# Optimization experiments

Measured on AMD Instinct MI355X. Metric: run time of the kernel, lower is better.

Reference implementation:

```python
import jax, jax.numpy as jnp
import numpy as np

_MAX_SQRT_GRADIENT = 1000.0
NUM_HEADS = 16


@jax.custom_vjp
def sqrt_bound(x):
    return jnp.sqrt(x)

def _sb_fwd(x):
    return jnp.sqrt(x), x

def _sb_bwd(x, g):
    return (g / jnp.sqrt(jnp.clip(4.0 * x, 1.0 / _MAX_SQRT_GRADIENT**2)),)

sqrt_bound.defvjp(_sb_fwd, _sb_bwd)


def block_diag_linear(x, w):
    # x: [..., H*I], w: [H, I, J]
    H, I, J = w.shape
    xb = x.reshape(x.shape[:-1] + (H, I))
    y = jnp.einsum('bshi,hij->bshj', xb, w)
    return y.reshape(x.shape[:-1] + (H * J,))


def self_att_pool(h, num_heads):
    # h: [B, S, D]; attention over S, then max over S with keepdims
    n_state = h.shape[-1] // num_heads
    scores = jnp.matmul(h, jnp.swapaxes(h, -2, -1)) * (1.0 / np.sqrt(n_state))
    attn = jax.nn.softmax(scores, axis=-1)              # [B, S, S]
    pooled = jnp.matmul(attn, h)                        # [B, S, D]
    return jnp.max(pooled, axis=-2, keepdims=True)      # [B, 1, D]


def setup_inputs() -> dict:
    key = jax.random.key(0)
    k1, k2, k3, k4 = jax.random.split(key, 4)
    B, S, D = 4, 4096, 2048
    H = NUM_HEADS
    bw = D // H  # 128
    std = np.sqrt(1.0 / bw)
    x = jax.random.normal(k1, (B, S, D), dtype=jnp.float32)
    h = jax.random.normal(k2, (B, S, D), dtype=jnp.float32)
    w_in = jax.random.normal(k3, (H, bw, bw), dtype=jnp.float32) * std
    w_a = jax.random.normal(k4, (H, bw, bw), dtype=jnp.float32) * std
    # rnn_param_init: uniform in [min_r^2+eps, max_r^2+eps], 0.5*log, then softplus-inverse of -t
    rng = np.random.default_rng(0)
    eps = 1e-8
    u = rng.uniform(0.9**2 + eps, 0.999**2 + eps, size=(D,)).astype(np.float32)
    t = 0.5 * np.log(u)
    a_param = jnp.asarray(np.log(np.exp(-t) - 1.0).astype(np.float32))
    return {"x": x, "h": h, "w_in": w_in, "w_a": w_a, "a_param": a_param}


def reference(x, h, w_in, w_a, a_param):
    gate_x = jax.nn.sigmoid(block_diag_linear(x, w_in))
    gate_a = jax.nn.sigmoid(block_diag_linear(x, w_a))
    log_a = -8.0 * jax.nn.softplus(a_param) * gate_a     # [B, S, D]
    a = jnp.exp(log_a)
    gated_x = x * gate_x
    normalized_x = gated_x * sqrt_bound(1.0 - jnp.exp(2.0 * log_a))
    h_pooled = self_att_pool(h, NUM_HEADS)               # [B, 1, D]
    return a * h_pooled + normalized_x
```

## Files before the change

kernel.cpp:

```cpp
#include <hip/hip_runtime.h>
#include <hip/hip_bf16.h>
#include <cstdint>

typedef _Float16 f16;
typedef _Float16 f16x4 __attribute__((ext_vector_type(4)));
typedef _Float16 f16x8 __attribute__((ext_vector_type(8)));
typedef float f32x4 __attribute__((ext_vector_type(4)));

#define B_ 4
#define S_ 4096
#define D_ 2048
#define NH 16
#define BW 128

__global__ __launch_bounds__(256) void cvt_kernel(const float* __restrict__ h,
                                                  f16* __restrict__ hf,
                                                  f16* __restrict__ hT) {
    __shared__ f16 tile[64][72];
    int s0 = blockIdx.y * 64;
    int d0 = blockIdx.x * 64;
    int tid = threadIdx.x;
    int r  = tid >> 4;
    int c4 = (tid & 15) * 4;
    #pragma unroll
    for (int rr = r; rr < 64; rr += 16) {
        f32x4 v = *(const f32x4*)(h + (size_t)(s0 + rr) * D_ + d0 + c4);
        f16x4 o;
        o[0] = (f16)v[0]; o[1] = (f16)v[1]; o[2] = (f16)v[2]; o[3] = (f16)v[3];
        *(f16x4*)(hf + (size_t)(s0 + rr) * D_ + d0 + c4) = o;
        tile[rr][c4 + 0] = o[0]; tile[rr][c4 + 1] = o[1];
        tile[rr][c4 + 2] = o[2]; tile[rr][c4 + 3] = o[3];
    }
    __syncthreads();
    #pragma unroll
    for (int dd = r; dd < 64; dd += 16) {
        f16x4 o;
        o[0] = tile[c4 + 0][dd]; o[1] = tile[c4 + 1][dd];
        o[2] = tile[c4 + 2][dd]; o[3] = tile[c4 + 3][dd];
        *(f16x4*)(hT + (size_t)(d0 + dd) * S_ + s0 + c4) = o;
    }
}

__device__ __forceinline__ unsigned f2ord(float f) {
    unsigned u = __float_as_uint(f);
    return (u & 0x80000000u) ? ~u : (u | 0x80000000u);
}

template<int EPI>
__global__ __launch_bounds__(256) void gemm_nt(const f16* __restrict__ A,
                                               const f16* __restrict__ Bm,
                                               float* __restrict__ C,
                                               unsigned* __restrict__ hp,
                                               int M, int N, int K, float alpha) {
    __shared__ f16 lA[128 * 32];
    __shared__ f16 lB[128 * 32];
    int tid  = threadIdx.x;
    int m0   = blockIdx.y * 128;
    int n0   = blockIdx.x * 128;
    int wave = tid >> 6;
    int lane = tid & 63;
    int wr   = (wave >> 1) * 64;
    int wc   = (wave & 1) * 64;
    int l15  = lane & 15;
    int quad = lane >> 4;

    const f16* aSrc = A + (size_t)(m0 + (tid >> 2)) * K + (tid & 3) * 8;
    const f16* bSrc = Bm + (size_t)(n0 + (tid >> 2)) * K + (tid & 3) * 8;
    size_t rowStep = (size_t)64 * K;

    f32x4 acc[4][4];
    #pragma unroll
    for (int i = 0; i < 4; i++)
        #pragma unroll
        for (int j = 0; j < 4; j++) acc[i][j] = (f32x4)0.0f;

    for (int k0 = 0; k0 < K; k0 += 32) {
        __builtin_amdgcn_global_load_lds(
            (const __attribute__((address_space(1))) void*)(aSrc),
            (__attribute__((address_space(3))) void*)(lA + tid * 8), 16, 0, 0);
        __builtin_amdgcn_global_load_lds(
            (const __attribute__((address_space(1))) void*)(aSrc + rowStep),
            (__attribute__((address_space(3))) void*)(lA + 2048 + tid * 8), 16, 0, 0);
        __builtin_amdgcn_global_load_lds(
            (const __attribute__((address_space(1))) void*)(bSrc),
            (__attribute__((address_space(3))) void*)(lB + tid * 8), 16, 0, 0);
        __builtin_amdgcn_global_load_lds(
            (const __attribute__((address_space(1))) void*)(bSrc + rowStep),
            (__attribute__((address_space(3))) void*)(lB + 2048 + tid * 8), 16, 0, 0);
        __syncthreads();

        f16x8 af[4], bf[4];
        #pragma unroll
        for (int i = 0; i < 4; i++) {
            af[i] = *(const f16x8*)(lA + (wr + i * 16 + l15) * 32 + quad * 8);
            bf[i] = *(const f16x8*)(lB + (wc + i * 16 + l15) * 32 + quad * 8);
        }
        #pragma unroll
        for (int i = 0; i < 4; i++)
            #pragma unroll
            for (int j = 0; j < 4; j++)
                acc[i][j] = __builtin_amdgcn_mfma_f32_16x16x32_f16(af[i], bf[j], acc[i][j], 0, 0, 0);
        __syncthreads();
        aSrc += 32; bSrc += 32;
    }

    if (EPI == 0) {
        #pragma unroll
        for (int i = 0; i < 4; i++) {
            int row = m0 + wr + i * 16 + quad * 4;
            #pragma unroll
            for (int j = 0; j < 4; j++) {
                int col = n0 + wc + j * 16 + l15;
                float* cp = C + (size_t)row * N + col;
                #pragma unroll
                for (int r = 0; r < 4; r++) cp[(size_t)r * N] = alpha * acc[i][j][r];
            }
        }
    } else {
        #pragma unroll
        for (int j = 0; j < 4; j++) {
            int col = n0 + wc + j * 16 + l15;
            float m = acc[0][j][0];
            #pragma unroll
            for (int i = 0; i < 4; i++)
                #pragma unroll
                for (int r = 0; r < 4; r++) m = fmaxf(m, acc[i][j][r]);
            atomicMax(hp + col, f2ord(m));
        }
    }
}

__global__ __launch_bounds__(256) void softmax_kernel(const float* __restrict__ scores,
                                                      f16* __restrict__ attn) {
    int row = blockIdx.x;
    int tid = threadIdx.x;
    const float* src = scores + (size_t)row * S_;
    f32x4 v[4];
    float m = -3.4e38f;
    #pragma unroll
    for (int j = 0; j < 4; j++) {
        v[j] = *(const f32x4*)(src + tid * 4 + j * 1024);
        #pragma unroll
        for (int e = 0; e < 4; e++) m = fmaxf(m, v[j][e]);
    }
    #pragma unroll
    for (int o = 32; o > 0; o >>= 1) m = fmaxf(m, __shfl_xor(m, o, 64));
    __shared__ float sm[4];
    __shared__ float ss[4];
    int wave = tid >> 6, lane = tid & 63;
    if (lane == 0) sm[wave] = m;
    __syncthreads();
    m = fmaxf(fmaxf(sm[0], sm[1]), fmaxf(sm[2], sm[3]));
    float sum = 0.f;
    #pragma unroll
    for (int j = 0; j < 4; j++)
        #pragma unroll
        for (int e = 0; e < 4; e++) { v[j][e] = __expf(v[j][e] - m); sum += v[j][e]; }
    #pragma unroll
    for (int o = 32; o > 0; o >>= 1) sum += __shfl_xor(sum, o, 64);
    if (lane == 0) ss[wave] = sum;
    __syncthreads();
    sum = ss[0] + ss[1] + ss[2] + ss[3];
    float inv = 1.0f / sum;
    f16* dst = attn + (size_t)row * S_;
    #pragma unroll
    for (int j = 0; j < 4; j++) {
        f16x4 o;
        #pragma unroll
        for (int e = 0; e < 4; e++) o[e] = (f16)(v[j][e] * inv);
        *(f16x4*)(dst + tid * 4 + j * 1024) = o;
    }
}

__global__ __launch_bounds__(256, 2) void final_kernel(const float* __restrict__ x,
                                                       const float* __restrict__ w_in,
                                                       const float* __restrict__ w_a,
                                                       const float* __restrict__ a_param,
                                                       const unsigned* __restrict__ hp_u,
                                                       float* __restrict__ out) {
    __shared__ float xs[8 * 2048];
    int wg = blockIdx.x;
    int b  = wg >> 9;
    int s0 = (wg & 511) * 8;
    int tid = threadIdx.x;
    const float* xbase = x + ((size_t)b * S_ + s0) * D_;
    {
        int r  = tid >> 5;
        int c0 = (tid & 31) * 4;
        #pragma unroll
        for (int it = 0; it < 16; it++) {
            int c = c0 + it * 128;
            *(f32x4*)(xs + r * 2048 + c) = *(const f32x4*)(xbase + (size_t)r * D_ + c);
        }
    }
    __syncthreads();

    int hd = tid >> 4;
    int j0 = (tid & 15) * 8;
    const float* wi  = w_in + hd * (BW * BW) + j0;
    const float* wa  = w_a  + hd * (BW * BW) + j0;
    const float* xsh = xs + hd * 128;

    float accx[8][8], acca[8][8];
    #pragma unroll
    for (int jj = 0; jj < 8; jj++)
        #pragma unroll
        for (int r = 0; r < 8; r++) { accx[jj][r] = 0.f; acca[jj][r] = 0.f; }

    for (int i = 0; i < 128; i += 4) {
        f32x4 xr[8];
        #pragma unroll
        for (int r = 0; r < 8; r++) xr[r] = *(const f32x4*)(xsh + r * 2048 + i);
        #pragma unroll
        for (int k = 0; k < 4; k++) {
            f32x4 wv0 = *(const f32x4*)(wi + (i + k) * 128);
            f32x4 wv1 = *(const f32x4*)(wi + (i + k) * 128 + 4);
            f32x4 wa0 = *(const f32x4*)(wa + (i + k) * 128);
            f32x4 wa1 = *(const f32x4*)(wa + (i + k) * 128 + 4);
            #pragma unroll
            for (int jj = 0; jj < 8; jj++) {
                float wiv = (jj < 4) ? wv0[jj] : wv1[jj - 4];
                float wav = (jj < 4) ? wa0[jj] : wa1[jj - 4];
                #pragma unroll
                for (int r = 0; r < 8; r++) {
                    accx[jj][r] = fmaf(xr[r][k], wiv, accx[jj][r]);
                    acca[jj][r] = fmaf(xr[r][k], wav, acca[jj][r]);
                }
            }
        }
    }

    float n8sp[8], hpv[8];
    #pragma unroll
    for (int jj = 0; jj < 8; jj++) {
        int d = hd * 128 + j0 + jj;
        n8sp[jj] = -8.f * log1pf(__expf(a_param[d]));
        unsigned u = hp_u[b * D_ + d];
        unsigned bits = (u >> 31) ? (u ^ 0x80000000u) : ~u;
        hpv[jj] = __uint_as_float(bits);
    }
    float* obase = out + ((size_t)b * S_ + s0) * D_ + hd * 128 + j0;
    #pragma unroll
    for (int r = 0; r < 8; r++) {
        f32x4 o0, o1;
        #pragma unroll
        for (int jj = 0; jj < 8; jj++) {
            float gx = 1.f / (1.f + __expf(-accx[jj][r]));
            float ga = 1.f / (1.f + __expf(-acca[jj][r]));
            float a  = __expf(n8sp[jj] * ga);
            float ns = sqrtf(fmaxf(1.f - a * a, 0.f));
            float xv = xs[r * 2048 + hd * 128 + j0 + jj];
            float val = a * hpv[jj] + xv * gx * ns;
            if (jj < 4) o0[jj] = val; else o1[jj - 4] = val;
        }
        *(f32x4*)(obase + (size_t)r * D_) = o0;
        *(f32x4*)(obase + (size_t)r * D_ + 4) = o1;
    }
}

extern "C" void kernel_launch(void* const* d_in, const int* in_sizes, int n_in,
                              void* d_out, int out_size, void* d_ws, size_t ws_size,
                              hipStream_t stream) {
    const float* x       = (const float*)d_in[0];
    const float* h       = (const float*)d_in[1];
    const float* w_in    = (const float*)d_in[2];
    const float* w_a     = (const float*)d_in[3];
    const float* a_param = (const float*)d_in[4];
    float* out = (float*)d_out;

    char* ws = (char*)d_ws;
    f16*      hf     = (f16*)ws;
    f16*      hT     = (f16*)(ws + ((size_t)16 << 20));
    float*    scores = (float*)(ws + ((size_t)32 << 20));
    f16*      attn   = (f16*)(ws + ((size_t)96 << 20));
    unsigned* hp     = (unsigned*)(ws + ((size_t)128 << 20));

    hipMemsetAsync(hp, 0, (size_t)B_ * D_ * sizeof(unsigned), stream);

    const float scale = 0.08838834764831845f;
    for (int b = 0; b < B_; b++) {
        const f16* hfc = hf;
        const f16* hTc = hT;
        const float* hb = h + (size_t)b * S_ * D_;
        cvt_kernel<<<dim3(D_ / 64, S_ / 64), 256, 0, stream>>>(hb, hf, hT);
        gemm_nt<0><<<dim3(S_ / 128, S_ / 128), 256, 0, stream>>>(
            hfc, hfc, scores, nullptr, S_, S_, D_, scale);
        softmax_kernel<<<dim3(S_), 256, 0, stream>>>(scores, attn);
        gemm_nt<1><<<dim3(D_ / 128, S_ / 128), 256, 0, stream>>>(
            attn, hTc, nullptr, hp + b * D_, S_, D_, S_, 1.0f);
    }
    final_kernel<<<dim3((B_ * S_) / 8), 256, 0, stream>>>(x, w_in, w_a, a_param, hp, out);
}
```

Before: 1.541 ms.

## Move gate projections to MFMA and store attention scores in fp16

Replaces the fp32 FMA block-diagonal gate kernel with an MFMA kernel. It stages pre-transposed fp16 weights, prepared once per call, and fp16-converted x tiles in LDS, one workgroup per 256 rows and one head. Separately, the QK^T GEMM now writes fp16 scores and softmax reads them, halving the traffic of the large scores buffer. The cost is lower precision: x is rounded to fp16 both for the gates and for the output term, the scores lose precision, and the new epilogue's per-element stores are less vectorized.

```diff
diff --git a/kernel.cpp b/kernel.cpp
--- a/kernel.cpp
+++ b/kernel.cpp
@@ -41,6 +41,24 @@
     }
 }
 
+__global__ __launch_bounds__(256) void prep_wT(const float* __restrict__ w,
+                                               f16* __restrict__ wT) {
+    int hd = blockIdx.x;
+    const float* src = w + hd * 16384;
+    f16* dst = wT + hd * 16384;
+    int tid = threadIdx.x;
+    int j0 = (tid & 31) * 4;
+    #pragma unroll
+    for (int p = 0; p < 16; p++) {
+        int i = (tid >> 5) + p * 8;
+        f32x4 v = *(const f32x4*)(src + i * 128 + j0);
+        int kc = i >> 5, il = i & 31;
+        #pragma unroll
+        for (int e = 0; e < 4; e++)
+            dst[kc * 4096 + (j0 + e) * 32 + il] = (f16)v[e];
+    }
+}
+
 __device__ __forceinline__ unsigned f2ord(float f) {
     unsigned u = __float_as_uint(f);
     return (u & 0x80000000u) ? ~u : (u | 0x80000000u);
@@ -49,7 +67,7 @@
 template<int EPI>
 __global__ __launch_bounds__(256) void gemm_nt(const f16* __restrict__ A,
                                                const f16* __restrict__ Bm,
-                                               float* __restrict__ C,
+                                               void* __restrict__ C,
                                                unsigned* __restrict__ hp,
                                                int M, int N, int K, float alpha) {
     __shared__ f16 lA[128 * 32];
@@ -105,15 +123,16 @@
     }
 
     if (EPI == 0) {
+        f16* Cf = (f16*)C;
         #pragma unroll
         for (int i = 0; i < 4; i++) {
             int row = m0 + wr + i * 16 + quad * 4;
             #pragma unroll
             for (int j = 0; j < 4; j++) {
                 int col = n0 + wc + j * 16 + l15;
-                float* cp = C + (size_t)row * N + col;
+                f16* cp = Cf + (size_t)row * N + col;
                 #pragma unroll
-                for (int r = 0; r < 4; r++) cp[(size_t)r * N] = alpha * acc[i][j][r];
+                for (int r = 0; r < 4; r++) cp[(size_t)r * N] = (f16)(alpha * acc[i][j][r]);
             }
         }
     } else {
@@ -130,19 +149,21 @@
     }
 }
 
-__global__ __launch_bounds__(256) void softmax_kernel(const float* __restrict__ scores,
+__global__ __launch_bounds__(256) void softmax_kernel(const f16* __restrict__ scores,
                                                       f16* __restrict__ attn) {
     int row = blockIdx.x;
     int tid = threadIdx.x;
-    const float* src = scores + (size_t)row * S_;
-    f32x4 v[4];
+    const f16* src = scores + (size_t)row * S_;
+    float v[16];
+    #pragma unroll
+    for (int j = 0; j < 2; j++) {
+        f16x8 raw = *(const f16x8*)(src + tid * 8 + j * 2048);
+        #pragma unroll
+        for (int e = 0; e < 8; e++) v[j * 8 + e] = (float)raw[e];
+    }
     float m = -3.4e38f;
     #pragma unroll
-    for (int j = 0; j < 4; j++) {
-        v[j] = *(const f32x4*)(src + tid * 4 + j * 1024);
-        #pragma unroll
-        for (int e = 0; e < 4; e++) m = fmaxf(m, v[j][e]);
-    }
+    for (int e = 0; e < 16; e++) m = fmaxf(m, v[e]);
     #pragma unroll
     for (int o = 32; o > 0; o >>= 1) m = fmaxf(m, __shfl_xor(m, o, 64));
     __shared__ float sm[4];
@@ -153,9 +174,7 @@
     m = fmaxf(fmaxf(sm[0], sm[1]), fmaxf(sm[2], sm[3]));
     float sum = 0.f;
     #pragma unroll
-    for (int j = 0; j < 4; j++)
-        #pragma unroll
-        for (int e = 0; e < 4; e++) { v[j][e] = __expf(v[j][e] - m); sum += v[j][e]; }
+    for (int e = 0; e < 16; e++) { v[e] = __expf(v[e] - m); sum += v[e]; }
     #pragma unroll
     for (int o = 32; o > 0; o >>= 1) sum += __shfl_xor(sum, o, 64);
     if (lane == 0) ss[wave] = sum;
@@ -164,97 +183,111 @@
     float inv = 1.0f / sum;
     f16* dst = attn + (size_t)row * S_;
     #pragma unroll
+    for (int j = 0; j < 2; j++) {
+        f16x8 o;
+        #pragma unroll
+        for (int e = 0; e < 8; e++) o[e] = (f16)(v[j * 8 + e] * inv);
+        *(f16x8*)(dst + tid * 8 + j * 2048) = o;
+    }
+}
+
+__global__ __launch_bounds__(512, 1) void final2_kernel(
+    const float* __restrict__ x, const f16* __restrict__ wTi,
+    const f16* __restrict__ wTa, const float* __restrict__ a_param,
+    const unsigned* __restrict__ hp_u, float* __restrict__ out) {
+    __shared__ f16 xs[4 * 256 * 32];
+    __shared__ f16 lwi[16384];
+    __shared__ f16 lwa[16384];
+    int tid  = threadIdx.x;
+    int hd   = blockIdx.y;
+    int row0 = blockIdx.x * 256;
+    int b    = row0 >> 12;
+    int wave = tid >> 6, lane = tid & 63;
+
+    const f16* wsi = wTi + hd * 16384;
+    const f16* wsa = wTa + hd * 16384;
+    #pragma unroll
+    for (int c = 0; c < 4; c++) {
+        int off = (wave * 4 + c) * 512 + lane * 8;
+        __builtin_amdgcn_global_load_lds(
+            (const __attribute__((address_space(1))) void*)(wsi + off),
+            (__attribute__((address_space(3))) void*)(lwi + off), 16, 0, 0);
+        __builtin_amdgcn_global_load_lds(
+            (const __attribute__((address_space(1))) void*)(wsa + off),
+            (__attribute__((address_space(3))) void*)(lwa + off), 16, 0, 0);
+    }
+
+    {
+        int rr   = tid >> 4;
+        int col8 = (tid & 15) * 8;
+        int kc = col8 >> 5, cl = col8 & 31;
+        const float* xb = x + (size_t)row0 * D_ + hd * 128;
+        #pragma unroll
+        for (int it = 0; it < 8; it++) {
+            int row = it * 32 + rr;
+            f32x4 v0 = *(const f32x4*)(xb + (size_t)row * D_ + col8);
+            f32x4 v1 = *(const f32x4*)(xb + (size_t)row * D_ + col8 + 4);
+            f16x8 o;
+            o[0] = (f16)v0[0]; o[1] = (f16)v0[1]; o[2] = (f16)v0[2]; o[3] = (f16)v0[3];
+            o[4] = (f16)v1[0]; o[5] = (f16)v1[1]; o[6] = (f16)v1[2]; o[7] = (f16)v1[3];
+            *(f16x8*)(xs + kc * 8192 + row * 32 + cl) = o;
+        }
+    }
+    __syncthreads();
+
+    int wr = (wave >> 1) * 64;
+    int wc = (wave & 1) * 64;
+    int l15 = lane & 15, quad = lane >> 4;
+
+    f32x4 ai[4][4], aa[4][4];
+    #pragma unroll
+    for (int i = 0; i < 4; i++)
+        #pragma unroll
+        for (int j = 0; j < 4; j++) { ai[i][j] = (f32x4)0.0f; aa[i][j] = (f32x4)0.0f; }
+
+    #pragma unroll
+    for (int ks = 0; ks < 4; ks++) {
+        f16x8 af[4], bi[4], ba[4];
+        #pragma unroll
+        for (int i = 0; i < 4; i++)
+            af[i] = *(const f16x8*)(xs + ks * 8192 + (wr + i * 16 + l15) * 32 + quad * 8);
+        #pragma unroll
+        for (int j = 0; j < 4; j++) {
+            bi[j] = *(const f16x8*)(lwi + ks * 4096 + (wc + j * 16 + l15) * 32 + quad * 8);
+            ba[j] = *(const f16x8*)(lwa + ks * 4096 + (wc + j * 16 + l15) * 32 + quad * 8);
+        }
+        #pragma unroll
+        for (int i = 0; i < 4; i++)
+            #pragma unroll
+            for (int j = 0; j < 4; j++) {
+                ai[i][j] = __builtin_amdgcn_mfma_f32_16x16x32_f16(af[i], bi[j], ai[i][j], 0, 0, 0);
+                aa[i][j] = __builtin_amdgcn_mfma_f32_16x16x32_f16(af[i], ba[j], aa[i][j], 0, 0, 0);
+            }
+    }
+
+    #pragma unroll
     for (int j = 0; j < 4; j++) {
-        f16x4 o;
-        #pragma unroll
-        for (int e = 0; e < 4; e++) o[e] = (f16)(v[j][e] * inv);
-        *(f16x4*)(dst + tid * 4 + j * 1024) = o;
-    }
-}
-
-__global__ __launch_bounds__(256, 2) void final_kernel(const float* __restrict__ x,
-                                                       const float* __restrict__ w_in,
-                                                       const float* __restrict__ w_a,
-                                                       const float* __restrict__ a_param,
-                                                       const unsigned* __restrict__ hp_u,
-                                                       float* __restrict__ out) {
-    __shared__ float xs[8 * 2048];
-    int wg = blockIdx.x;
-    int b  = wg >> 9;
-    int s0 = (wg & 511) * 8;
-    int tid = threadIdx.x;
-    const float* xbase = x + ((size_t)b * S_ + s0) * D_;
-    {
-        int r  = tid >> 5;
-        int c0 = (tid & 31) * 4;
-        #pragma unroll
-        for (int it = 0; it < 16; it++) {
-            int c = c0 + it * 128;
-            *(f32x4*)(xs + r * 2048 + c) = *(const f32x4*)(xbase + (size_t)r * D_ + c);
-        }
-    }
-    __syncthreads();
-
-    int hd = tid >> 4;
-    int j0 = (tid & 15) * 8;
-    const float* wi  = w_in + hd * (BW * BW) + j0;
-    const float* wa  = w_a  + hd * (BW * BW) + j0;
-    const float* xsh = xs + hd * 128;
-
-    float accx[8][8], acca[8][8];
-    #pragma unroll
-    for (int jj = 0; jj < 8; jj++)
-        #pragma unroll
-        for (int r = 0; r < 8; r++) { accx[jj][r] = 0.f; acca[jj][r] = 0.f; }
-
-    for (int i = 0; i < 128; i += 4) {
-        f32x4 xr[8];
-        #pragma unroll
-        for (int r = 0; r < 8; r++) xr[r] = *(const f32x4*)(xsh + r * 2048 + i);
-        #pragma unroll
-        for (int k = 0; k < 4; k++) {
-            f32x4 wv0 = *(const f32x4*)(wi + (i + k) * 128);
-            f32x4 wv1 = *(const f32x4*)(wi + (i + k) * 128 + 4);
-            f32x4 wa0 = *(const f32x4*)(wa + (i + k) * 128);
-            f32x4 wa1 = *(const f32x4*)(wa + (i + k) * 128 + 4);
-            #pragma unroll
-            for (int jj = 0; jj < 8; jj++) {
-                float wiv = (jj < 4) ? wv0[jj] : wv1[jj - 4];
-                float wav = (jj < 4) ? wa0[jj] : wa1[jj - 4];
-                #pragma unroll
-                for (int r = 0; r < 8; r++) {
-                    accx[jj][r] = fmaf(xr[r][k], wiv, accx[jj][r]);
-                    acca[jj][r] = fmaf(xr[r][k], wav, acca[jj][r]);
-                }
-            }
-        }
-    }
-
-    float n8sp[8], hpv[8];
-    #pragma unroll
-    for (int jj = 0; jj < 8; jj++) {
-        int d = hd * 128 + j0 + jj;
-        n8sp[jj] = -8.f * log1pf(__expf(a_param[d]));
+        int n = wc + j * 16 + l15;
+        int d = hd * 128 + n;
+        float n8sp = -8.f * log1pf(__expf(a_param[d]));
         unsigned u = hp_u[b * D_ + d];
         unsigned bits = (u >> 31) ? (u ^ 0x80000000u) : ~u;
-        hpv[jj] = __uint_as_float(bits);
-    }
-    float* obase = out + ((size_t)b * S_ + s0) * D_ + hd * 128 + j0;
-    #pragma unroll
-    for (int r = 0; r < 8; r++) {
-        f32x4 o0, o1;
-        #pragma unroll
-        for (int jj = 0; jj < 8; jj++) {
-            float gx = 1.f / (1.f + __expf(-accx[jj][r]));
-            float ga = 1.f / (1.f + __expf(-acca[jj][r]));
-            float a  = __expf(n8sp[jj] * ga);
-            float ns = sqrtf(fmaxf(1.f - a * a, 0.f));
-            float xv = xs[r * 2048 + hd * 128 + j0 + jj];
-            float val = a * hpv[jj] + xv * gx * ns;
-            if (jj < 4) o0[jj] = val; else o1[jj - 4] = val;
-        }
-        *(f32x4*)(obase + (size_t)r * D_) = o0;
-        *(f32x4*)(obase + (size_t)r * D_ + 4) = o1;
+        float hpv = __uint_as_float(bits);
+        int xc = (n >> 5) * 8192 + (n & 31);
+        #pragma unroll
+        for (int i = 0; i < 4; i++) {
+            int mbase = wr + i * 16 + quad * 4;
+            #pragma unroll
+            for (int r = 0; r < 4; r++) {
+                int m = mbase + r;
+                float gx = 1.f / (1.f + __expf(-ai[i][j][r]));
+                float ga = 1.f / (1.f + __expf(-aa[i][j][r]));
+                float a  = __expf(n8sp * ga);
+                float ns = sqrtf(fmaxf(1.f - a * a, 0.f));
+                float xv = (float)xs[xc + m * 32];
+                out[(size_t)(row0 + m) * D_ + d] = a * hpv + xv * gx * ns;
+            }
+        }
     }
 }
 
@@ -271,23 +304,26 @@
     char* ws = (char*)d_ws;
     f16*      hf     = (f16*)ws;
     f16*      hT     = (f16*)(ws + ((size_t)16 << 20));
-    float*    scores = (float*)(ws + ((size_t)32 << 20));
-    f16*      attn   = (f16*)(ws + ((size_t)96 << 20));
-    unsigned* hp     = (unsigned*)(ws + ((size_t)128 << 20));
+    f16*      scores = (f16*)(ws + ((size_t)32 << 20));
+    f16*      attn   = (f16*)(ws + ((size_t)64 << 20));
+    unsigned* hp     = (unsigned*)(ws + ((size_t)96 << 20));
+    f16*      wTi    = (f16*)(ws + ((size_t)96 << 20) + (64 << 10));
+    f16*      wTa    = (f16*)(ws + ((size_t)96 << 20) + (64 << 10) + (512 << 10));
 
     hipMemsetAsync(hp, 0, (size_t)B_ * D_ * sizeof(unsigned), stream);
+    prep_wT<<<dim3(16), 256, 0, stream>>>(w_in, wTi);
+    prep_wT<<<dim3(16), 256, 0, stream>>>(w_a, wTa);
 
     const float scale = 0.08838834764831845f;
     for (int b = 0; b < B_; b++) {
-        const f16* hfc = hf;
-        const f16* hTc = hT;
         const float* hb = h + (size_t)b * S_ * D_;
         cvt_kernel<<<dim3(D_ / 64, S_ / 64), 256, 0, stream>>>(hb, hf, hT);
         gemm_nt<0><<<dim3(S_ / 128, S_ / 128), 256, 0, stream>>>(
-            hfc, hfc, scores, nullptr, S_, S_, D_, scale);
+            hf, hf, (void*)scores, nullptr, S_, S_, D_, scale);
         softmax_kernel<<<dim3(S_), 256, 0, stream>>>(scores, attn);
         gemm_nt<1><<<dim3(D_ / 128, S_ / 128), 256, 0, stream>>>(
-            attn, hTc, nullptr, hp + b * D_, S_, D_, S_, 1.0f);
-    }
-    final_kernel<<<dim3((B_ * S_) / 8), 256, 0, stream>>>(x, w_in, w_a, a_param, hp, out);
-}
+            attn, hT, nullptr, hp + b * D_, S_, D_, S_, 1.0f);
+    }
+    final2_kernel<<<dim3((B_ * S_) / 256, NH), 512, 0, stream>>>(
+        x, wTi, wTa, a_param, hp, out);
+}
```

New measurement: 1.400 ms. -9.1%, faster.
